# Kernel optimization log

Measured on AMD Instinct MI355X. Metric: run time of the kernel, lower is better.

Reference implementation:

```python
import jax, jax.numpy as jnp
import numpy as np

E, B, D, T = 8, 4096, 2048, 2048
H = D // 2 + T // 2  # expert hidden dim = 2048
TOP_K = 2


def setup_inputs() -> dict:
    key = jax.random.key(0)
    ks = jax.random.split(key, 5)
    s_in = 1.0 / np.sqrt(D)
    s_h = 1.0 / np.sqrt(H)
    return {
        "xs": jax.random.normal(ks[0], (E, B, D), dtype=jnp.float32),
        "Wg": jax.random.normal(ks[1], (D,), dtype=jnp.float32) * s_in,
        "bg": jnp.zeros((1,), dtype=jnp.float32),
        "W1": jax.random.normal(ks[2], (E, D, H), dtype=jnp.float32) * s_in,
        "b1": jnp.zeros((E, H), dtype=jnp.float32),
        "W2": jax.random.normal(ks[3], (E, H, T), dtype=jnp.float32) * s_h,
        "b2": jnp.zeros((E, T), dtype=jnp.float32),
    }


def reference(xs, Wg, bg, W1, b1, W2, b2):
    # Gating: logits[b, e] = x[e][b] @ Wg + bg  -> [B, E]
    logits = jnp.einsum("ebd,d->be", xs, Wg) + bg
    probs = jax.nn.softmax(logits, axis=1)
    top_k_values, top_k_indices = jax.lax.top_k(probs, TOP_K)  # [B, K]

    # Dense expert compute over each expert's own input stream.
    # hidden[e, b, h] = relu(x[e] @ W1[e] + b1[e]); out[e, b, t] = hidden @ W2[e] + b2[e]
    hidden = jax.nn.relu(jnp.einsum("ebd,edh->ebh", xs, W1) + b1[:, None, :])
    expert_out = jnp.einsum("ebh,eht->ebt", hidden, W2) + b2[:, None, :]  # [E, B, T]

    # Gather the top-k experts per token. In the original, masked-dense compute
    # + output mask is mathematically identical to this gather.
    per_token = jnp.transpose(expert_out, (1, 0, 2))  # [B, E, T]
    selected = jnp.take_along_axis(per_token, top_k_indices[:, :, None], axis=1)  # [B, K, T]

    out = jnp.sum(top_k_values[:, :, None] * selected, axis=1)  # [B, T]
    return out, top_k_values
```

## Files before the change

### kernel.cpp

```cpp
#include <hip/hip_runtime.h>
#include <hip/hip_bf16.h>
#include <stdint.h>

#define E_ 8
#define B_ 4096
#define D_ 2048
#define T_ 2048
#define H_ 2048
#define KDIM 2048
#define NDIM 2048
#define ECAP 2048
#define NROWS (E_ * 1024 + 256)

typedef __attribute__((ext_vector_type(4))) float f32x4;
typedef __attribute__((ext_vector_type(8))) unsigned short u16x8;
typedef __attribute__((ext_vector_type(8))) __bf16 bf16x8;

__device__ __forceinline__ unsigned short f2bf(float f) {
    __hip_bfloat16 h = __float2bfloat16(f);
    return __builtin_bit_cast(unsigned short, h);
}

__device__ __forceinline__ void gload_lds16(const void* g, void* lds) {
    __builtin_amdgcn_global_load_lds(
        (const __attribute__((address_space(1))) void*)g,
        (__attribute__((address_space(3))) void*)lds, 16, 0, 0);
}

__global__ __launch_bounds__(256) void fused_pre(
    const float* __restrict__ xs, const float* __restrict__ Wg,
    const float* __restrict__ bg,
    const float* __restrict__ W1, const float* __restrict__ W2,
    unsigned short* __restrict__ Wt1, unsigned short* __restrict__ Wt2,
    float* __restrict__ out_topk, int* __restrict__ counts,
    unsigned short* __restrict__ Axf, int* __restrict__ tokf,
    float* __restrict__ probf, int nwt)
{
    const int bid = blockIdx.x;
    const int t = threadIdx.x;

    if (bid < nwt) {
        const int z   = bid >> 10;
        const int rem = bid & 1023;
        const int kb  = ((rem >> 5) & 31) << 6;
        const int nb  = (rem & 31) << 6;
        const int e   = z & 7;
        const float* W = (z >> 3) ? W2 : W1;
        unsigned short* Wt = (z >> 3) ? Wt2 : Wt1;

        __shared__ float tile[64][68];
        const float* src = W + ((size_t)e * KDIM + kb) * NDIM + nb;
        {
            const int kr = t >> 2, nc = (t & 3) * 16;
            #pragma unroll
            for (int j = 0; j < 4; ++j) {
                f32x4 v = __builtin_nontemporal_load(
                    (const f32x4*)(src + (size_t)kr * NDIM + nc + j * 4));
                *(f32x4*)&tile[kr][nc + j * 4] = v;
            }
        }
        __syncthreads();
        {
            const int nn = t >> 2, kc = (t & 3) * 16;
            unsigned short wbuf[16];
            #pragma unroll
            for (int j = 0; j < 16; ++j) wbuf[j] = f2bf(tile[kc + j][nn]);
            unsigned short* dst =
                Wt + ((size_t)e * NDIM + nb + nn) * KDIM + kb + kc;
            *(u16x8*)dst       = *(const u16x8*)&wbuf[0];
            *((u16x8*)dst + 1) = *(const u16x8*)&wbuf[8];
        }
        return;
    }

    const int b = bid - nwt;
    const int wave = t >> 6, lane = t & 63;
    __shared__ float red[E_][4];
    __shared__ int sh_i0, sh_i1, sh_p0, sh_p1;

    const f32x4 wg0 = ((const f32x4*)Wg)[t];
    const f32x4 wg1 = ((const f32x4*)Wg)[t + 256];

    f32x4 xa[E_], xb[E_];
    #pragma unroll
    for (int e = 0; e < E_; ++e) {
        const f32x4* xr = (const f32x4*)(xs + ((size_t)e * B_ + b) * D_);
        xa[e] = __builtin_nontemporal_load(&xr[t]);
        xb[e] = __builtin_nontemporal_load(&xr[t + 256]);
        float p = xa[e].x*wg0.x + xa[e].y*wg0.y + xa[e].z*wg0.z + xa[e].w*wg0.w
                + xb[e].x*wg1.x + xb[e].y*wg1.y + xb[e].z*wg1.z + xb[e].w*wg1.w;
        #pragma unroll
        for (int off = 32; off >= 1; off >>= 1) p += __shfl_xor(p, off);
        if (lane == 0) red[e][wave] = p;
    }
    __syncthreads();
    if (t == 0) {
        float pr[E_];
        float mx = -3.0e38f;
        #pragma unroll
        for (int e = 0; e < E_; ++e) {
            pr[e] = red[e][0] + red[e][1] + red[e][2] + red[e][3] + bg[0];
            mx = fmaxf(mx, pr[e]);
        }
        float s = 0.f;
        #pragma unroll
        for (int e = 0; e < E_; ++e) { pr[e] = expf(pr[e] - mx); s += pr[e]; }
        float inv = 1.0f / s;
        #pragma unroll
        for (int e = 0; e < E_; ++e) pr[e] *= inv;
        int i0 = 0;
        #pragma unroll
        for (int e = 1; e < E_; ++e) if (pr[e] > pr[i0]) i0 = e;
        int i1 = (i0 == 0) ? 1 : 0;
        #pragma unroll
        for (int e = 0; e < E_; ++e) { if (e != i0 && pr[e] > pr[i1]) i1 = e; }
        float p0 = pr[i0], p1 = pr[i1];
        out_topk[2*b]   = p0;
        out_topk[2*b+1] = p1;
        int pos0 = atomicAdd(&counts[i0], 1);
        int pos1 = atomicAdd(&counts[i1], 1);
        if (pos0 >= ECAP) pos0 = ECAP - 1;
        if (pos1 >= ECAP) pos1 = ECAP - 1;
        tokf[i0 * ECAP + pos0] = b;  probf[i0 * ECAP + pos0] = p0;
        tokf[i1 * ECAP + pos1] = b;  probf[i1 * ECAP + pos1] = p1;
        sh_i0 = i0; sh_i1 = i1; sh_p0 = pos0; sh_p1 = pos1;
    }
    __syncthreads();
    const int i0 = sh_i0, i1 = sh_i1;
    f32x4 s0a = xa[0], s0b = xb[0], s1a = xa[0], s1b = xb[0];
    #pragma unroll
    for (int e = 0; e < E_; ++e) {
        if (i0 == e) { s0a = xa[e]; s0b = xb[e]; }
        if (i1 == e) { s1a = xa[e]; s1b = xb[e]; }
    }
    unsigned short* r0 = Axf + (size_t)(i0 * ECAP + sh_p0) * D_;
    unsigned short* r1 = Axf + (size_t)(i1 * ECAP + sh_p1) * D_;
    r0[4*t+0]=f2bf(s0a.x); r0[4*t+1]=f2bf(s0a.y); r0[4*t+2]=f2bf(s0a.z); r0[4*t+3]=f2bf(s0a.w);
    r0[1024+4*t+0]=f2bf(s0b.x); r0[1024+4*t+1]=f2bf(s0b.y); r0[1024+4*t+2]=f2bf(s0b.z); r0[1024+4*t+3]=f2bf(s0b.w);
    r1[4*t+0]=f2bf(s1a.x); r1[4*t+1]=f2bf(s1a.y); r1[4*t+2]=f2bf(s1a.z); r1[4*t+3]=f2bf(s1a.w);
    r1[1024+4*t+0]=f2bf(s1b.x); r1[1024+4*t+1]=f2bf(s1b.y); r1[1024+4*t+2]=f2bf(s1b.z); r1[1024+4*t+3]=f2bf(s1b.w);
}

__global__ void build_tiles(const int* __restrict__ counts,
                            int* __restrict__ tiles, int* __restrict__ ebase)
{
    if (threadIdx.x == 0 && blockIdx.x == 0) {
        int n = 0, base = 0;
        for (int e = 0; e < E_; ++e) {
            ebase[e] = base;
            int c = counts[e]; if (c > ECAP) c = ECAP;
            int te = (c + 255) >> 8;
            for (int m = 0; m < te; ++m) tiles[1 + n++] = (e << 16) | m;
            base += c;
        }
        tiles[0] = n;
    }
}

__global__ __launch_bounds__(256) void wtrans1(
    const float* __restrict__ W, unsigned short* __restrict__ Wt)
{
    const int e  = blockIdx.z;
    const int kb = blockIdx.x * 64;
    const int nb = blockIdx.y * 64;
    const int t  = threadIdx.x;
    __shared__ float tile[64][68];

    const float* src = W + ((size_t)e * KDIM + kb) * NDIM + nb;
    {
        const int kr = t >> 2, nc = (t & 3) * 16;
        #pragma unroll
        for (int j = 0; j < 4; ++j) {
            f32x4 v = __builtin_nontemporal_load(
                (const f32x4*)(src + (size_t)kr * NDIM + nc + j * 4));
            *(f32x4*)&tile[kr][nc + j * 4] = v;
        }
    }
    __syncthreads();
    {
        const int nn = t >> 2, kc = (t & 3) * 16;
        unsigned short wbuf[16];
        #pragma unroll
        for (int j = 0; j < 16; ++j) wbuf[j] = f2bf(tile[kc + j][nn]);
        unsigned short* dst = Wt + ((size_t)e * NDIM + nb + nn) * KDIM + kb + kc;
        *(u16x8*)dst       = *(const u16x8*)&wbuf[0];
        *((u16x8*)dst + 1) = *(const u16x8*)&wbuf[8];
    }
}

#define BAR  __builtin_amdgcn_s_barrier()

template<int LAYER>
__global__ __launch_bounds__(1024, 4) void moe_gemm(
    const unsigned short* __restrict__ Abuf,
    const unsigned short* __restrict__ Wt,
    const float* __restrict__ bias,
    const int* __restrict__ counts,
    const int* __restrict__ tiles,
    const int* __restrict__ ebase,
    const int* __restrict__ tokf,
    const float* __restrict__ probf,
    unsigned short* __restrict__ hidden_out,
    float* __restrict__ out)
{
    const int nMt = tiles[0];
    const int bid = blockIdx.x;
    const int mt  = bid >> 3;
    const int np  = bid & 7;
    if (mt >= nMt) return;
    const int info = tiles[1 + mt];
    const int e    = info >> 16;
    const int mloc = (info & 0xffff) * 256;
    const int arow0 = (LAYER == 1) ? (e * ECAP + mloc) : (ebase[e] + mloc);
    const int n0   = np * 256;
    int n_e = counts[e]; if (n_e > ECAP) n_e = ECAP;

    const int t = threadIdx.x;
    const int lane = t & 63;
    const int w = t >> 6;
    const int wm = (w >> 2) * 64;
    const int wn = (w & 3) * 64;
    const int lg = lane >> 4;

    __shared__ u16x8 As[4 * 1024];
    __shared__ u16x8 Bs[4 * 1024];

    const int ksw = (((t & 3) ^ ((t >> 3) & 3)) << 3);
    const unsigned short* aptr = Abuf + (size_t)(arow0 + (t >> 2)) * KDIM + ksw;
    const unsigned short* bptr =
        Wt + ((size_t)e * NDIM + n0 + (t >> 2)) * KDIM + ksw;

#define STG(BUF, KT) do{ \
    gload_lds16(aptr + (KT)*32, &As[(BUF)*1024 + w*64]); \
    gload_lds16(bptr + (KT)*32, &Bs[(BUF)*1024 + w*64]); }while(0)

    f32x4 acc[4][4];
    #pragma unroll
    for (int i = 0; i < 4; ++i)
        #pragma unroll
        for (int j = 0; j < 4; ++j) {
            f32x4 z = {0.f, 0.f, 0.f, 0.f};
            acc[i][j] = z;
        }

    STG(0, 0); STG(1, 1); STG(2, 2);

    const int usw = (lane >> 1) & 3;
    for (int kt = 0; kt < 64; ++kt) {
        asm volatile("s_waitcnt vmcnt(4)" ::: "memory");
        BAR;
        int tn = kt + 3; if (tn > 63) tn = 63;
        STG((kt + 3) & 3, tn);

        const int base = (kt & 3) * 1024;
        bf16x8 af[4];
        #pragma unroll
        for (int mi = 0; mi < 4; ++mi) {
            const int row = wm + mi * 16 + (lane & 15);
            af[mi] = __builtin_bit_cast(bf16x8, As[base + row * 4 + (lg ^ usw)]);
        }
        #pragma unroll
        for (int ni = 0; ni < 4; ++ni) {
            const int row = wn + ni * 16 + (lane & 15);
            bf16x8 bq = __builtin_bit_cast(bf16x8, Bs[base + row * 4 + (lg ^ usw)]);
            #pragma unroll
            for (int mi = 0; mi < 4; ++mi)
                acc[mi][ni] = __builtin_amdgcn_mfma_f32_16x16x32_bf16(
                    af[mi], bq, acc[mi][ni], 0, 0, 0);
        }
    }
    asm volatile("s_waitcnt vmcnt(0)" ::: "memory");

    #pragma unroll
    for (int mi = 0; mi < 4; ++mi) {
        #pragma unroll
        for (int rr = 0; rr < 4; ++rr) {
            const int rloc = wm + mi * 16 + ((lane >> 4) << 2) + rr;
            if (mloc + rloc >= n_e) continue;
            #pragma unroll
            for (int ni = 0; ni < 4; ++ni) {
                const int col = n0 + wn + ni * 16 + (lane & 15);
                float v = acc[mi][ni][rr];
                if (LAYER == 1) {
                    v += bias[e * NDIM + col];
                    v = fmaxf(v, 0.f);
                    hidden_out[(size_t)(ebase[e] + mloc + rloc) * H_ + col] = f2bf(v);
                } else {
                    const int f = e * ECAP + mloc + rloc;
                    v = (v + bias[e * NDIM + col]) * probf[f];
                    atomicAdd(&out[(size_t)tokf[f] * T_ + col], v);
                }
            }
        }
    }
#undef STG
}

extern "C" void kernel_launch(void* const* d_in, const int* in_sizes, int n_in,
                              void* d_out, int out_size, void* d_ws, size_t ws_size,
                              hipStream_t stream)
{
    const float* xs = (const float*)d_in[0];
    const float* Wg = (const float*)d_in[1];
    const float* bg = (const float*)d_in[2];
    const float* W1 = (const float*)d_in[3];
    const float* b1 = (const float*)d_in[4];
    const float* W2 = (const float*)d_in[5];
    const float* b2 = (const float*)d_in[6];

    float* out      = (float*)d_out;
    float* out_topk = out + (size_t)B_ * T_;

    char* ws = (char*)d_ws;
    int*   counts = (int*)ws;
    int*   tiles  = (int*)(ws + 256);
    int*   ebase  = (int*)(ws + 768);
    int*   tokf   = (int*)(ws + 1024);
    float* probf  = (float*)(ws + 1024 + E_ * ECAP * 4);
    size_t off = 1024 + (size_t)E_ * ECAP * 8;
    off = (off + 255) & ~(size_t)255;
    unsigned short* Axf    = (unsigned short*)(ws + off); off += (size_t)E_ * ECAP * D_ * 2;
    unsigned short* hidden = (unsigned short*)(ws + off); off += (size_t)NROWS * H_ * 2;
    unsigned short* Wt1    = (unsigned short*)(ws + off); off += (size_t)E_ * KDIM * NDIM * 2;
    size_t off_big = off + (size_t)E_ * KDIM * NDIM * 2;
    unsigned short* Wt2 = (unsigned short*)(ws + off);

    const bool big = (ws_size >= off_big);

    hipMemsetAsync(counts, 0, 256, stream);
    hipMemsetAsync(out, 0, (size_t)B_ * T_ * sizeof(float), stream);

    dim3 blk(256), gblk(1024);
    dim3 ggrid(39 * 8);

    if (big) {
        const int nwt = 16 * 1024;
        fused_pre<<<dim3(nwt + B_), blk, 0, stream>>>(
            xs, Wg, bg, W1, W2, Wt1, Wt2, out_topk, counts, Axf, tokf, probf, nwt);
        build_tiles<<<dim3(1), dim3(64), 0, stream>>>(counts, tiles, ebase);
        moe_gemm<1><<<ggrid, gblk, 0, stream>>>(
            Axf, Wt1, b1, counts, tiles, ebase, tokf, probf, hidden, nullptr);
        moe_gemm<2><<<ggrid, gblk, 0, stream>>>(
            hidden, Wt2, b2, counts, tiles, ebase, tokf, probf, nullptr, out);
    } else {
        dim3 tgrid(32, 32, E_);
        fused_pre<<<dim3(B_), blk, 0, stream>>>(
            xs, Wg, bg, W1, W2, Wt1, Wt1, out_topk, counts, Axf, tokf, probf, 0);
        build_tiles<<<dim3(1), dim3(64), 0, stream>>>(counts, tiles, ebase);
        wtrans1<<<tgrid, blk, 0, stream>>>(W1, Wt1);
        moe_gemm<1><<<ggrid, gblk, 0, stream>>>(
            Axf, Wt1, b1, counts, tiles, ebase, tokf, probf, hidden, nullptr);
        wtrans1<<<tgrid, blk, 0, stream>>>(W2, Wt1);
        moe_gemm<2><<<ggrid, gblk, 0, stream>>>(
            hidden, Wt1, b2, counts, tiles, ebase, tokf, probf, nullptr, out);
    }
}
```

Baseline: 498.9 us.

## Swizzle transpose LDS tile, reorder fused_pre blocks, group GEMM tiles for L2 reuse

XOR-swizzles the shared-memory transpose tile columns by row group to reduce bank conflicts on the column-wise read. Reorders fused_pre so the token gating blocks come first and the weight-transpose blocks follow. Remaps moe_gemm block indices so groups of eight M-tiles share an N-panel in adjacent blocks, aiming for better L2 reuse of weights. The GEMM grid is padded to a multiple of 64 blocks, which adds a few early-exit blocks.

```diff
diff --git a/kernel.cpp b/kernel.cpp
--- a/kernel.cpp
+++ b/kernel.cpp
@@ -34,14 +34,15 @@
     unsigned short* __restrict__ Wt1, unsigned short* __restrict__ Wt2,
     float* __restrict__ out_topk, int* __restrict__ counts,
     unsigned short* __restrict__ Axf, int* __restrict__ tokf,
-    float* __restrict__ probf, int nwt)
+    float* __restrict__ probf)
 {
     const int bid = blockIdx.x;
     const int t = threadIdx.x;
 
-    if (bid < nwt) {
-        const int z   = bid >> 10;
-        const int rem = bid & 1023;
+    if (bid >= B_) {
+        const int wb  = bid - B_;
+        const int z   = wb >> 10;
+        const int rem = wb & 1023;
         const int kb  = ((rem >> 5) & 31) << 6;
         const int nb  = (rem & 31) << 6;
         const int e   = z & 7;
@@ -52,11 +53,12 @@
         const float* src = W + ((size_t)e * KDIM + kb) * NDIM + nb;
         {
             const int kr = t >> 2, nc = (t & 3) * 16;
+            const int sw = (kr >> 4) << 2;
             #pragma unroll
             for (int j = 0; j < 4; ++j) {
                 f32x4 v = __builtin_nontemporal_load(
                     (const f32x4*)(src + (size_t)kr * NDIM + nc + j * 4));
-                *(f32x4*)&tile[kr][nc + j * 4] = v;
+                *(f32x4*)&tile[kr][(nc + j * 4) ^ sw] = v;
             }
         }
         __syncthreads();
@@ -64,7 +66,10 @@
             const int nn = t >> 2, kc = (t & 3) * 16;
             unsigned short wbuf[16];
             #pragma unroll
-            for (int j = 0; j < 16; ++j) wbuf[j] = f2bf(tile[kc + j][nn]);
+            for (int j = 0; j < 16; ++j) {
+                const int r = kc + j;
+                wbuf[j] = f2bf(tile[r][nn ^ ((r >> 4) << 2)]);
+            }
             unsigned short* dst =
                 Wt + ((size_t)e * NDIM + nb + nn) * KDIM + kb + kc;
             *(u16x8*)dst       = *(const u16x8*)&wbuf[0];
@@ -73,7 +78,7 @@
         return;
     }
 
-    const int b = bid - nwt;
+    const int b = bid;
     const int wave = t >> 6, lane = t & 63;
     __shared__ float red[E_][4];
     __shared__ int sh_i0, sh_i1, sh_p0, sh_p1;
@@ -169,11 +174,12 @@
     const float* src = W + ((size_t)e * KDIM + kb) * NDIM + nb;
     {
         const int kr = t >> 2, nc = (t & 3) * 16;
+        const int sw = (kr >> 4) << 2;
         #pragma unroll
         for (int j = 0; j < 4; ++j) {
             f32x4 v = __builtin_nontemporal_load(
                 (const f32x4*)(src + (size_t)kr * NDIM + nc + j * 4));
-            *(f32x4*)&tile[kr][nc + j * 4] = v;
+            *(f32x4*)&tile[kr][(nc + j * 4) ^ sw] = v;
         }
     }
     __syncthreads();
@@ -181,7 +187,10 @@
         const int nn = t >> 2, kc = (t & 3) * 16;
         unsigned short wbuf[16];
         #pragma unroll
-        for (int j = 0; j < 16; ++j) wbuf[j] = f2bf(tile[kc + j][nn]);
+        for (int j = 0; j < 16; ++j) {
+            const int r = kc + j;
+            wbuf[j] = f2bf(tile[r][nn ^ ((r >> 4) << 2)]);
+        }
         unsigned short* dst = Wt + ((size_t)e * NDIM + nb + nn) * KDIM + kb + kc;
         *(u16x8*)dst       = *(const u16x8*)&wbuf[0];
         *((u16x8*)dst + 1) = *(const u16x8*)&wbuf[8];
@@ -205,8 +214,11 @@
 {
     const int nMt = tiles[0];
     const int bid = blockIdx.x;
-    const int mt  = bid >> 3;
-    const int np  = bid & 7;
+    const int x    = bid & 7;
+    const int rest = bid >> 3;
+    const int np   = rest & 7;
+    const int mtg  = rest >> 3;
+    const int mt   = mtg * 8 + x;
     if (mt >= nMt) return;
     const int info = tiles[1 + mt];
     const int e    = info >> 16;
@@ -331,12 +343,12 @@
     hipMemsetAsync(out, 0, (size_t)B_ * T_ * sizeof(float), stream);
 
     dim3 blk(256), gblk(1024);
-    dim3 ggrid(39 * 8);
+    dim3 ggrid(((39 + 7) / 8) * 64);
 
     if (big) {
         const int nwt = 16 * 1024;
-        fused_pre<<<dim3(nwt + B_), blk, 0, stream>>>(
-            xs, Wg, bg, W1, W2, Wt1, Wt2, out_topk, counts, Axf, tokf, probf, nwt);
+        fused_pre<<<dim3(B_ + nwt), blk, 0, stream>>>(
+            xs, Wg, bg, W1, W2, Wt1, Wt2, out_topk, counts, Axf, tokf, probf);
         build_tiles<<<dim3(1), dim3(64), 0, stream>>>(counts, tiles, ebase);
         moe_gemm<1><<<ggrid, gblk, 0, stream>>>(
             Axf, Wt1, b1, counts, tiles, ebase, tokf, probf, hidden, nullptr);
@@ -345,7 +357,7 @@
     } else {
         dim3 tgrid(32, 32, E_);
         fused_pre<<<dim3(B_), blk, 0, stream>>>(
-            xs, Wg, bg, W1, W2, Wt1, Wt1, out_topk, counts, Axf, tokf, probf, 0);
+            xs, Wg, bg, W1, W2, Wt1, Wt1, out_topk, counts, Axf, tokf, probf);
         build_tiles<<<dim3(1), dim3(64), 0, stream>>>(counts, tiles, ebase);
         wtrans1<<<tgrid, blk, 0, stream>>>(W1, Wt1);
         moe_gemm<1><<<ggrid, gblk, 0, stream>>>(
```

After: 516.6 us. 3.5% more time.
